# Kernel tuning notes

Measured on AMD Instinct MI355X. Metric: run time of the kernel, lower is better.

## Reference

```python
import jax, jax.numpy as jnp
import numpy as np

RATIO = 0.95
EPS = 1e-8
BIDIRECTIONAL = True


def _normalize_desc(fmap):
    # fmap: [1, ch, h, w] -> [h*w, ch], L2-normalized rows
    ch = fmap.shape[1]
    d = fmap.reshape(ch, -1).T
    return d / jnp.sqrt(jnp.sum(jnp.square(d), axis=1, keepdims=True))


def setup_inputs() -> dict:
    key = jax.random.key(0)
    k1, k2 = jax.random.split(key)
    map_A = jax.random.normal(k1, (1, 512, 96, 128), dtype=jnp.float32)
    map_B = jax.random.normal(k2, (1, 512, 96, 128), dtype=jnp.float32)
    return {"map_A": map_A, "map_B": map_B}


def reference(map_A, map_B):
    d1 = _normalize_desc(map_A)  # [N1, ch]
    d2 = _normalize_desc(map_B)  # [N2, ch]

    sim = d1 @ d2.T  # [N1, N2]

    # A -> B: top-2 over columns
    nns_sim12, nns12 = jax.lax.top_k(sim, 2)
    nns_dist12 = 2.0 - 2.0 * nns_sim12
    ratios12 = nns_dist12[:, 0] / (nns_dist12[:, 1] + EPS)
    nn12 = nns12[:, 0]
    match_sim = nns_sim12[:, 0]

    # B -> A: top-2 over rows of sim (columns of sim.T)
    nns_sim21, nns21 = jax.lax.top_k(sim.T, 2)
    nns_dist21 = 2.0 - 2.0 * nns_sim21
    ratios21 = nns_dist21[:, 0] / (nns_dist21[:, 1] + EPS)
    nn21 = nns21[:, 0]
    if not BIDIRECTIONAL:
        ratios21 = ratios21 * 0.0

    ids1 = jnp.arange(sim.shape[0])
    mask = (ids1 == nn21[nn12]) & (ratios12 <= RATIO) & (ratios21[nn12] <= RATIO)

    masked_sim = jnp.where(mask, match_sim, 0.0)
    return masked_sim, nn12, mask
```

## Files before the change

### kernel.cpp

```cpp
#include <hip/hip_runtime.h>
#include <stdint.h>

#define N      12288
#define CH     512
#define NTILE  96
#define NS     8
#define JT_PER_S 12
#define GPJ    16
#define NSTEP  (JT_PER_S * GPJ)

typedef _Float16 f16x8 __attribute__((ext_vector_type(8)));
typedef float    f32x4 __attribute__((ext_vector_type(4)));

struct Top2 { float v0, v1; int i0, i1; };

__device__ float g_invA[N];
__device__ float g_invB[N];
__device__ unsigned short g_AT[(size_t)N * 1024];
__device__ unsigned short g_BT[(size_t)N * 1024];
__device__ Top2  g_rpart[NS][N];
__device__ Top2  g_cpart[NTILE][N];
__device__ int   g_nn12[N];
__device__ float g_r12[N];
__device__ float g_sim0[N];
__device__ int   g_nn21[N];
__device__ float g_r21[N];

__device__ __forceinline__ void t2_ins(float v, int idx,
                                       float& v0, int& i0, float& v1, int& i1) {
  bool beats0 = (v > v0) || (v == v0 && idx < i0);
  bool beats1 = (v > v1) || (v == v1 && idx < i1);
  if (beats0) { v1 = v0; i1 = i0; v0 = v; i0 = idx; }
  else if (beats1) { v1 = v; i1 = idx; }
}

__device__ __forceinline__ float bf16_quant(float f) {
  unsigned int u = __float_as_uint(f);
  unsigned int r = 0x7fffu + ((u >> 16) & 1u);
  unsigned int q = ((u + r) >> 16) << 16;
  return __uint_as_float(q);
}

__global__ __launch_bounds__(256)
void prep_kernel(const float* __restrict__ A, const float* __restrict__ B) {
  const int d0 = blockIdx.x * 64;
  const float* src = blockIdx.y ? B : A;
  unsigned short* dst = blockIdx.y ? g_BT : g_AT;
  float* inv = blockIdx.y ? g_invB : g_invA;

  __shared__ float Ls[32][68];
  __shared__ unsigned short Os[64][64];
  __shared__ float Ps[4][64];

  const int t = threadIdx.x;
  const int a = t >> 6, dl = t & 63;
  float sum = 0.f;

  for (int g = 0; g < 16; ++g) {
    __syncthreads();
    {
      const int c = t >> 3, dc = (t & 7) * 8;
      const float* p = src + (size_t)(g * 32 + c) * N + d0 + dc;
      float4 v0 = *reinterpret_cast<const float4*>(p);
      float4 v1 = *reinterpret_cast<const float4*>(p + 4);
      *reinterpret_cast<float4*>(&Ls[c][dc])     = v0;
      *reinterpret_cast<float4*>(&Ls[c][dc + 4]) = v1;
    }
    __syncthreads();
    {
      _Float16 hv[8] __attribute__((aligned(16)));
      _Float16 lv[8] __attribute__((aligned(16)));
#pragma unroll
      for (int j = 0; j < 8; ++j) {
        float v = Ls[a * 8 + j][dl] * 1024.0f;
        sum += v * v;
        _Float16 h = (_Float16)v;
        float rr = v - (float)h;
        hv[j] = h;
        lv[j] = (_Float16)rr;
      }
      *reinterpret_cast<uint4*>(&Os[dl][a * 8])      = *reinterpret_cast<const uint4*>(hv);
      *reinterpret_cast<uint4*>(&Os[dl][32 + a * 8]) = *reinterpret_cast<const uint4*>(lv);
    }
    __syncthreads();
    {
#pragma unroll
      for (int p2 = 0; p2 < 2; ++p2) {
        const int d = p2 * 32 + (t >> 3), ch = t & 7;
        const int sc = ch ^ (d & 7);
        *reinterpret_cast<uint4*>((char*)dst
            + ((size_t)g * N + d0 + d) * 128 + sc * 16)
            = *reinterpret_cast<const uint4*>(&Os[d][ch * 8]);
      }
    }
  }
  Ps[a][dl] = sum;
  __syncthreads();
  if (t < 64) {
    float tot = Ps[0][t] + Ps[1][t] + Ps[2][t] + Ps[3][t];
    inv[d0 + t] = 1.0f / sqrtf(tot);
  }
}

__global__ __launch_bounds__(512, 4)
void sim_top2_mfma() {
  __shared__ unsigned short SM[2][2][128 * 64];
  __shared__ Top2 rowW[2][128];
  __shared__ Top2 colW[4][128];
  __shared__ float iaS[128];
  __shared__ float ibS[128];

  const int itile = blockIdx.x, slice = blockIdx.y;
  const int i0 = itile * 128;
  const int tid = threadIdx.x;
  const int wave = tid >> 6, lane = tid & 63;
  const int wr = wave & 3, wc = wave >> 2;
  const int fr = lane & 15, kq = lane >> 4;
  const int jtb = slice * JT_PER_S;

  const int tid2 = tid & 255;
  const char* opBase = (const char*)(wc ? g_BT : g_AT);

  uint4 s0, s1, s2, s3;
  auto issue = [&](int t) {
    const int gg = t & 15;
    const size_t rb = wc ? (size_t)(jtb + (t >> 4)) * 128 : (size_t)i0;
    const char* base = opBase + ((size_t)gg * N + rb) * 128 + tid2 * 16;
    s0 = *reinterpret_cast<const uint4*>(base);
    s1 = *reinterpret_cast<const uint4*>(base + 4096);
    s2 = *reinterpret_cast<const uint4*>(base + 8192);
    s3 = *reinterpret_cast<const uint4*>(base + 12288);
  };

  issue(0);

  if (tid < 128) {
    iaS[tid] = g_invA[i0 + tid];
    Top2 z; z.v0 = -1e30f; z.v1 = -1e30f; z.i0 = 0x7fffffff; z.i1 = 0x7fffffff;
    rowW[0][tid] = z; rowW[1][tid] = z;
  }

  const int f7 = fr & 7;
  const int cHi = (kq ^ f7) << 4;
  const int cLo = ((kq + 4) ^ f7) << 4;
  int aOff[2], bOff[4];
#pragma unroll
  for (int mi = 0; mi < 2; ++mi) aOff[mi] = (wr * 32 + mi * 16 + fr) * 128;
#pragma unroll
  for (int ni = 0; ni < 4; ++ni) bOff[ni] = (wc * 64 + ni * 16 + fr) * 128;

  char* const SMb = (char*)&SM[0][0][0];
  char* const wbase0 = SMb + wc * 16384 + tid2 * 16;

  int t = 0;
  for (int jt = jtb; jt < jtb + JT_PER_S; ++jt) {
    const int j0 = jt * 128;
    if (tid < 128) ibS[tid] = g_invB[j0 + tid];

    f32x4 acc[2][4];
#pragma unroll
    for (int mi = 0; mi < 2; ++mi)
#pragma unroll
      for (int ni = 0; ni < 4; ++ni)
#pragma unroll
        for (int q = 0; q < 4; ++q) acc[mi][ni][q] = 0.f;

    for (int g = 0; g < GPJ; ++g, ++t) {
      const int par = t & 1;
      __syncthreads();
      {
        char* wb = wbase0 + par * 32768;
        *reinterpret_cast<uint4*>(wb)          = s0;
        *reinterpret_cast<uint4*>(wb + 4096)   = s1;
        *reinterpret_cast<uint4*>(wb + 8192)   = s2;
        *reinterpret_cast<uint4*>(wb + 12288)  = s3;
      }
      if (t + 1 < NSTEP) issue(t + 1);
      __syncthreads();

      const char* bA = SMb + par * 32768;
      const char* bB = bA + 16384;
      f16x8 ah[2], al[2];
#pragma unroll
      for (int mi = 0; mi < 2; ++mi) {
        ah[mi] = *reinterpret_cast<const f16x8*>(bA + aOff[mi] + cHi);
        al[mi] = *reinterpret_cast<const f16x8*>(bA + aOff[mi] + cLo);
      }
#pragma unroll
      for (int ni = 0; ni < 4; ++ni) {
        f16x8 bh = *reinterpret_cast<const f16x8*>(bB + bOff[ni] + cHi);
        f16x8 bl = *reinterpret_cast<const f16x8*>(bB + bOff[ni] + cLo);
#pragma unroll
        for (int mi = 0; mi < 2; ++mi) {
          acc[mi][ni] = __builtin_amdgcn_mfma_f32_16x16x32_f16(ah[mi], bh, acc[mi][ni], 0, 0, 0);
          acc[mi][ni] = __builtin_amdgcn_mfma_f32_16x16x32_f16(ah[mi], bl, acc[mi][ni], 0, 0, 0);
          acc[mi][ni] = __builtin_amdgcn_mfma_f32_16x16x32_f16(al[mi], bh, acc[mi][ni], 0, 0, 0);
        }
      }
    }

    float ib[4];
#pragma unroll
    for (int ni = 0; ni < 4; ++ni) ib[ni] = ibS[wc * 64 + ni * 16 + fr];
#pragma unroll
    for (int mi = 0; mi < 2; ++mi)
#pragma unroll
      for (int r = 0; r < 4; ++r) {
        const float iar = iaS[wr * 32 + mi * 16 + kq * 4 + r];
#pragma unroll
        for (int ni = 0; ni < 4; ++ni)
          acc[mi][ni][r] *= iar * ib[ni];
      }

#pragma unroll
    for (int mi = 0; mi < 2; ++mi) {
#pragma unroll
      for (int r = 0; r < 4; ++r) {
        const int row = wr * 32 + mi * 16 + kq * 4 + r;
        float v0 = -1e30f, v1 = -1e30f; int id0 = 0x7fffffff, id1 = 0x7fffffff;
#pragma unroll
        for (int ni = 0; ni < 4; ++ni)
          t2_ins(acc[mi][ni][r], j0 + wc * 64 + ni * 16 + fr, v0, id0, v1, id1);
#pragma unroll
        for (int m = 1; m < 16; m <<= 1) {
          float ov0 = __shfl_xor(v0, m), ov1 = __shfl_xor(v1, m);
          int oi0 = __shfl_xor(id0, m), oi1 = __shfl_xor(id1, m);
          t2_ins(ov0, oi0, v0, id0, v1, id1);
          t2_ins(ov1, oi1, v0, id0, v1, id1);
        }
        if (fr == 0) {
          Top2 tT = rowW[wc][row];
          t2_ins(v0, id0, tT.v0, tT.i0, tT.v1, tT.i1);
          t2_ins(v1, id1, tT.v0, tT.i0, tT.v1, tT.i1);
          rowW[wc][row] = tT;
        }
      }
    }

#pragma unroll
    for (int ni = 0; ni < 4; ++ni) {
      float v0 = -1e30f, v1 = -1e30f; int id0 = 0x7fffffff, id1 = 0x7fffffff;
#pragma unroll
      for (int mi = 0; mi < 2; ++mi)
#pragma unroll
        for (int r = 0; r < 4; ++r)
          t2_ins(acc[mi][ni][r], i0 + wr * 32 + mi * 16 + kq * 4 + r, v0, id0, v1, id1);
#pragma unroll
      for (int m = 16; m < 64; m <<= 1) {
        float ov0 = __shfl_xor(v0, m), ov1 = __shfl_xor(v1, m);
        int oi0 = __shfl_xor(id0, m), oi1 = __shfl_xor(id1, m);
        t2_ins(ov0, oi0, v0, id0, v1, id1);
        t2_ins(ov1, oi1, v0, id0, v1, id1);
      }
      if (kq == 0) {
        Top2 tT; tT.v0 = v0; tT.v1 = v1; tT.i0 = id0; tT.i1 = id1;
        colW[wr][wc * 64 + ni * 16 + fr] = tT;
      }
    }
    __syncthreads();
    if (tid < 128) {
      Top2 tT = colW[0][tid];
#pragma unroll
      for (int w = 1; w < 4; ++w) {
        Top2 o = colW[w][tid];
        t2_ins(o.v0, o.i0, tT.v0, tT.i0, tT.v1, tT.i1);
        t2_ins(o.v1, o.i1, tT.v0, tT.i0, tT.v1, tT.i1);
      }
      g_cpart[itile][j0 + tid] = tT;
    }
  }

  __syncthreads();
  if (tid < 128) {
    Top2 tT = rowW[0][tid];
    Top2 o  = rowW[1][tid];
    t2_ins(o.v0, o.i0, tT.v0, tT.i0, tT.v1, tT.i1);
    t2_ins(o.v1, o.i1, tT.v0, tT.i0, tT.v1, tT.i1);
    g_rpart[slice][i0 + tid] = tT;
  }
}

__global__ void merge_kernel() {
  int i = blockIdx.x * 256 + threadIdx.x;
  if (i >= N) return;
  {
    float v0 = -1e30f, v1 = -1e30f; int id0 = 0x7fffffff, id1 = 0x7fffffff;
#pragma unroll
    for (int s = 0; s < NS; ++s) {
      Top2 p = g_rpart[s][i];
      t2_ins(p.v0, p.i0, v0, id0, v1, id1);
      t2_ins(p.v1, p.i1, v0, id0, v1, id1);
    }
    float d0 = 2.f - 2.f * v0, d1 = 2.f - 2.f * v1;
    g_nn12[i] = id0; g_r12[i] = d0 / (d1 + 1e-8f); g_sim0[i] = v0;
  }
  {
    float v0 = -1e30f, v1 = -1e30f; int id0 = 0x7fffffff, id1 = 0x7fffffff;
    for (int it = 0; it < NTILE; ++it) {
      Top2 p = g_cpart[it][i];
      t2_ins(p.v0, p.i0, v0, id0, v1, id1);
      t2_ins(p.v1, p.i1, v0, id0, v1, id1);
    }
    float d0 = 2.f - 2.f * v0, d1 = 2.f - 2.f * v1;
    g_nn21[i] = id0; g_r21[i] = d0 / (d1 + 1e-8f);
  }
}

__global__ void finalize_kernel(float* __restrict__ out) {
  int i = blockIdx.x * 256 + threadIdx.x;
  if (i >= N) return;
  int j = g_nn12[i];
  int jc = j < 0 ? 0 : (j >= N ? N - 1 : j);
  bool mask = (g_nn21[jc] == i) && (g_r12[i] <= 0.95f) && (g_r21[jc] <= 0.95f);
  out[i]         = bf16_quant(mask ? g_sim0[i] : 0.f);
  out[N + i]     = bf16_quant((float)j);
  out[2 * N + i] = mask ? 1.f : 0.f;
}

extern "C" void kernel_launch(void* const* d_in, const int* in_sizes, int n_in,
                              void* d_out, int out_size, void* d_ws, size_t ws_size,
                              hipStream_t stream) {
  const float* A = (const float*)d_in[0];
  const float* B = (const float*)d_in[1];
  (void)d_ws; (void)ws_size;

  prep_kernel<<<dim3(192, 2), 256, 0, stream>>>(A, B);
  sim_top2_mfma<<<dim3(NTILE, NS), 512, 0, stream>>>();
  merge_kernel<<<dim3((N + 255) / 256), 256, 0, stream>>>();
  finalize_kernel<<<dim3((N + 255) / 256), 256, 0, stream>>>((float*)d_out);
}
```

Baseline: 2.449 ms.

## Deepen global prefetch to two stages and remap blocks for L2 locality

Splits the register staging into two alternating sets so global loads for step t+2 are issued while step t is being consumed, which doubles the number of loads in flight. It replaces __syncthreads with raw s_barrier plus an explicit lgkmcnt wait so the barrier does not also wait on outstanding global loads. It also remaps block IDs so blocks that run together share A tiles and slices, to improve L2 reuse. In exchange the kernel holds extra VGPRs for the second staging set, which may reduce occupancy under the 512x4 launch bounds, and the hand-written barrier handling is easier to get wrong.

```diff
diff --git a/kernel.cpp b/kernel.cpp
--- a/kernel.cpp
+++ b/kernel.cpp
@@ -110,7 +110,9 @@
   __shared__ float iaS[128];
   __shared__ float ibS[128];
 
-  const int itile = blockIdx.x, slice = blockIdx.y;
+  const int bid = blockIdx.x + NTILE * blockIdx.y;
+  const int itile = (bid & 7) * 12 + ((bid >> 3) % 12);
+  const int slice = bid / NTILE;
   const int i0 = itile * 128;
   const int tid = threadIdx.x;
   const int wave = tid >> 6, lane = tid & 63;
@@ -121,24 +123,36 @@
   const int tid2 = tid & 255;
   const char* opBase = (const char*)(wc ? g_BT : g_AT);
 
-  uint4 s0, s1, s2, s3;
-  auto issue = [&](int t) {
+  uint4 sa0, sa1, sa2, sa3;
+  uint4 sb0, sb1, sb2, sb3;
+  auto issueA = [&](int t) {
     const int gg = t & 15;
     const size_t rb = wc ? (size_t)(jtb + (t >> 4)) * 128 : (size_t)i0;
     const char* base = opBase + ((size_t)gg * N + rb) * 128 + tid2 * 16;
-    s0 = *reinterpret_cast<const uint4*>(base);
-    s1 = *reinterpret_cast<const uint4*>(base + 4096);
-    s2 = *reinterpret_cast<const uint4*>(base + 8192);
-    s3 = *reinterpret_cast<const uint4*>(base + 12288);
+    sa0 = *reinterpret_cast<const uint4*>(base);
+    sa1 = *reinterpret_cast<const uint4*>(base + 4096);
+    sa2 = *reinterpret_cast<const uint4*>(base + 8192);
+    sa3 = *reinterpret_cast<const uint4*>(base + 12288);
   };
-
-  issue(0);
+  auto issueB = [&](int t) {
+    const int gg = t & 15;
+    const size_t rb = wc ? (size_t)(jtb + (t >> 4)) * 128 : (size_t)i0;
+    const char* base = opBase + ((size_t)gg * N + rb) * 128 + tid2 * 16;
+    sb0 = *reinterpret_cast<const uint4*>(base);
+    sb1 = *reinterpret_cast<const uint4*>(base + 4096);
+    sb2 = *reinterpret_cast<const uint4*>(base + 8192);
+    sb3 = *reinterpret_cast<const uint4*>(base + 12288);
+  };
 
   if (tid < 128) {
     iaS[tid] = g_invA[i0 + tid];
     Top2 z; z.v0 = -1e30f; z.v1 = -1e30f; z.i0 = 0x7fffffff; z.i1 = 0x7fffffff;
     rowW[0][tid] = z; rowW[1][tid] = z;
   }
+  __syncthreads();
+
+  issueA(0);
+  issueB(1);
 
   const int f7 = fr & 7;
   const int cHi = (kq ^ f7) << 4;
@@ -152,6 +166,44 @@
   char* const SMb = (char*)&SM[0][0][0];
   char* const wbase0 = SMb + wc * 16384 + tid2 * 16;
 
+#define KSTEP(PAR, S0, S1, S2, S3, ISSUE, TT)                                 \
+  {                                                                           \
+    __builtin_amdgcn_s_barrier();                                             \
+    asm volatile("" ::: "memory");                                            \
+    {                                                                         \
+      char* wb = wbase0 + (PAR) * 32768;                                      \
+      *reinterpret_cast<uint4*>(wb)         = S0;                             \
+      *reinterpret_cast<uint4*>(wb + 4096)  = S1;                             \
+      *reinterpret_cast<uint4*>(wb + 8192)  = S2;                             \
+      *reinterpret_cast<uint4*>(wb + 12288) = S3;                             \
+    }                                                                         \
+    if ((TT) + 2 < NSTEP) ISSUE((TT) + 2);                                    \
+    asm volatile("s_waitcnt lgkmcnt(0)" ::: "memory");                        \
+    __builtin_amdgcn_s_barrier();                                             \
+    asm volatile("" ::: "memory");                                            \
+    {                                                                         \
+      const char* bA = SMb + (PAR) * 32768;                                   \
+      const char* bB = bA + 16384;                                            \
+      f16x8 ah[2], al[2];                                                     \
+      _Pragma("unroll")                                                       \
+      for (int mi = 0; mi < 2; ++mi) {                                        \
+        ah[mi] = *reinterpret_cast<const f16x8*>(bA + aOff[mi] + cHi);        \
+        al[mi] = *reinterpret_cast<const f16x8*>(bA + aOff[mi] + cLo);        \
+      }                                                                       \
+      _Pragma("unroll")                                                       \
+      for (int ni = 0; ni < 4; ++ni) {                                        \
+        f16x8 bh = *reinterpret_cast<const f16x8*>(bB + bOff[ni] + cHi);      \
+        f16x8 bl = *reinterpret_cast<const f16x8*>(bB + bOff[ni] + cLo);      \
+        _Pragma("unroll")                                                     \
+        for (int mi = 0; mi < 2; ++mi) {                                      \
+          acc[mi][ni] = __builtin_amdgcn_mfma_f32_16x16x32_f16(ah[mi], bh, acc[mi][ni], 0, 0, 0); \
+          acc[mi][ni] = __builtin_amdgcn_mfma_f32_16x16x32_f16(ah[mi], bl, acc[mi][ni], 0, 0, 0); \
+          acc[mi][ni] = __builtin_amdgcn_mfma_f32_16x16x32_f16(al[mi], bh, acc[mi][ni], 0, 0, 0); \
+        }                                                                     \
+      }                                                                       \
+    }                                                                         \
+  }
+
   int t = 0;
   for (int jt = jtb; jt < jtb + JT_PER_S; ++jt) {
     const int j0 = jt * 128;
@@ -165,38 +217,11 @@
 #pragma unroll
         for (int q = 0; q < 4; ++q) acc[mi][ni][q] = 0.f;
 
-    for (int g = 0; g < GPJ; ++g, ++t) {
-      const int par = t & 1;
-      __syncthreads();
-      {
-        char* wb = wbase0 + par * 32768;
-        *reinterpret_cast<uint4*>(wb)          = s0;
-        *reinterpret_cast<uint4*>(wb + 4096)   = s1;
-        *reinterpret_cast<uint4*>(wb + 8192)   = s2;
-        *reinterpret_cast<uint4*>(wb + 12288)  = s3;
-      }
-      if (t + 1 < NSTEP) issue(t + 1);
-      __syncthreads();
-
-      const char* bA = SMb + par * 32768;
-      const char* bB = bA + 16384;
-      f16x8 ah[2], al[2];
-#pragma unroll
-      for (int mi = 0; mi < 2; ++mi) {
-        ah[mi] = *reinterpret_cast<const f16x8*>(bA + aOff[mi] + cHi);
-        al[mi] = *reinterpret_cast<const f16x8*>(bA + aOff[mi] + cLo);
-      }
-#pragma unroll
-      for (int ni = 0; ni < 4; ++ni) {
-        f16x8 bh = *reinterpret_cast<const f16x8*>(bB + bOff[ni] + cHi);
-        f16x8 bl = *reinterpret_cast<const f16x8*>(bB + bOff[ni] + cLo);
-#pragma unroll
-        for (int mi = 0; mi < 2; ++mi) {
-          acc[mi][ni] = __builtin_amdgcn_mfma_f32_16x16x32_f16(ah[mi], bh, acc[mi][ni], 0, 0, 0);
-          acc[mi][ni] = __builtin_amdgcn_mfma_f32_16x16x32_f16(ah[mi], bl, acc[mi][ni], 0, 0, 0);
-          acc[mi][ni] = __builtin_amdgcn_mfma_f32_16x16x32_f16(al[mi], bh, acc[mi][ni], 0, 0, 0);
-        }
-      }
+    for (int g2 = 0; g2 < GPJ / 2; ++g2) {
+      KSTEP(0, sa0, sa1, sa2, sa3, issueA, t);
+      ++t;
+      KSTEP(1, sb0, sb1, sb2, sb3, issueB, t);
+      ++t;
     }
 
     float ib[4];
@@ -269,6 +294,7 @@
       g_cpart[itile][j0 + tid] = tT;
     }
   }
+#undef KSTEP
 
   __syncthreads();
   if (tid < 128) {
```

Result: no change. 2.434 ms (-0.6%).

## Enlarge similarity GEMM tiles to 256x256 with dynamic shared memory

Applied to the files above, without the earlier changes.

Grows the per-block output tile from 128x128 to 256x256. Each wave now owns a 128x64 sub-tile with 32 accumulators, so every LDS fragment feeds more MFMAs and operand traffic per flop drops. The grid is rearranged to 48x16 with a swizzled itile order, shared memory moves to a 154 KB dynamic allocation, and the syncs become raw s_barrier calls with explicit lgkmcnt waits. In exchange, register pressure rises to 128 fp32 accumulators per lane, occupancy falls to launch_bounds 2, and there are fewer blocks to cover the CUs.

```diff
diff --git a/kernel.cpp b/kernel.cpp
--- a/kernel.cpp
+++ b/kernel.cpp
@@ -3,11 +3,13 @@
 
 #define N      12288
 #define CH     512
-#define NTILE  96
-#define NS     8
-#define JT_PER_S 12
+#define TI2    256
+#define NT2    48
+#define NS2    16
+#define JT2    3
 #define GPJ    16
-#define NSTEP  (JT_PER_S * GPJ)
+#define NSTEP2 (JT2 * GPJ)
+#define DSMEM_BYTES (131072 + 16384 + 8192 + 2048)
 
 typedef _Float16 f16x8 __attribute__((ext_vector_type(8)));
 typedef float    f32x4 __attribute__((ext_vector_type(4)));
@@ -18,8 +20,8 @@
 __device__ float g_invB[N];
 __device__ unsigned short g_AT[(size_t)N * 1024];
 __device__ unsigned short g_BT[(size_t)N * 1024];
-__device__ Top2  g_rpart[NS][N];
-__device__ Top2  g_cpart[NTILE][N];
+__device__ Top2  g_rpart[NS2][N];
+__device__ Top2  g_cpart[NT2][N];
 __device__ int   g_nn12[N];
 __device__ float g_r12[N];
 __device__ float g_sim0[N];
@@ -102,125 +104,143 @@
   }
 }
 
-__global__ __launch_bounds__(512, 4)
+__global__ __launch_bounds__(512, 2)
 void sim_top2_mfma() {
-  __shared__ unsigned short SM[2][2][128 * 64];
-  __shared__ Top2 rowW[2][128];
-  __shared__ Top2 colW[4][128];
-  __shared__ float iaS[128];
-  __shared__ float ibS[128];
-
-  const int itile = blockIdx.x, slice = blockIdx.y;
-  const int i0 = itile * 128;
+  extern __shared__ char smem[];
+  char* const SMb = smem;
+  Top2* const rowW = (Top2*)(smem + 131072);
+  Top2* const colW = (Top2*)(smem + 131072 + 16384);
+  float* const iaS = (float*)(smem + 131072 + 16384 + 8192);
+  float* const ibS = iaS + 256;
+
+  const int q = blockIdx.x;
+  const int itile = (q & 7) * 6 + (q >> 3);
+  const int slice = blockIdx.y;
+  const int i0 = itile * TI2;
   const int tid = threadIdx.x;
   const int wave = tid >> 6, lane = tid & 63;
-  const int wr = wave & 3, wc = wave >> 2;
+  const int wr = wave & 1, wc = wave >> 1;
   const int fr = lane & 15, kq = lane >> 4;
-  const int jtb = slice * JT_PER_S;
-
+  const int jtb = slice * JT2;
+
+  const int side = wave >> 2;
   const int tid2 = tid & 255;
-  const char* opBase = (const char*)(wc ? g_BT : g_AT);
-
-  uint4 s0, s1, s2, s3;
+  const char* opBase = (const char*)(side ? g_BT : g_AT);
+
+  uint4 s0, s1, s2, s3, s4, s5, s6, s7;
   auto issue = [&](int t) {
     const int gg = t & 15;
-    const size_t rb = wc ? (size_t)(jtb + (t >> 4)) * 128 : (size_t)i0;
+    const size_t rb = side ? (size_t)(jtb + (t >> 4)) * TI2 : (size_t)i0;
     const char* base = opBase + ((size_t)gg * N + rb) * 128 + tid2 * 16;
     s0 = *reinterpret_cast<const uint4*>(base);
     s1 = *reinterpret_cast<const uint4*>(base + 4096);
     s2 = *reinterpret_cast<const uint4*>(base + 8192);
     s3 = *reinterpret_cast<const uint4*>(base + 12288);
+    s4 = *reinterpret_cast<const uint4*>(base + 16384);
+    s5 = *reinterpret_cast<const uint4*>(base + 20480);
+    s6 = *reinterpret_cast<const uint4*>(base + 24576);
+    s7 = *reinterpret_cast<const uint4*>(base + 28672);
   };
 
   issue(0);
 
-  if (tid < 128) {
+  if (tid < 256) {
     iaS[tid] = g_invA[i0 + tid];
     Top2 z; z.v0 = -1e30f; z.v1 = -1e30f; z.i0 = 0x7fffffff; z.i1 = 0x7fffffff;
-    rowW[0][tid] = z; rowW[1][tid] = z;
-  }
+#pragma unroll
+    for (int w = 0; w < 4; ++w) rowW[w * 256 + tid] = z;
+  }
+  __syncthreads();
 
   const int f7 = fr & 7;
   const int cHi = (kq ^ f7) << 4;
   const int cLo = ((kq + 4) ^ f7) << 4;
-  int aOff[2], bOff[4];
-#pragma unroll
-  for (int mi = 0; mi < 2; ++mi) aOff[mi] = (wr * 32 + mi * 16 + fr) * 128;
-#pragma unroll
-  for (int ni = 0; ni < 4; ++ni) bOff[ni] = (wc * 64 + ni * 16 + fr) * 128;
-
-  char* const SMb = (char*)&SM[0][0][0];
-  char* const wbase0 = SMb + wc * 16384 + tid2 * 16;
+  const int aOff0 = (wr * 128 + fr) * 128;
+  const int bOff0 = (wc * 64 + fr) * 128;
+  char* const wbase0 = SMb + side * 32768 + tid2 * 16;
 
   int t = 0;
-  for (int jt = jtb; jt < jtb + JT_PER_S; ++jt) {
-    const int j0 = jt * 128;
-    if (tid < 128) ibS[tid] = g_invB[j0 + tid];
-
-    f32x4 acc[2][4];
-#pragma unroll
-    for (int mi = 0; mi < 2; ++mi)
+  for (int jt = jtb; jt < jtb + JT2; ++jt) {
+    const int j0 = jt * TI2;
+    if (tid < 256) ibS[tid] = g_invB[j0 + tid];
+
+    f32x4 acc[8][4];
+#pragma unroll
+    for (int mi = 0; mi < 8; ++mi)
 #pragma unroll
       for (int ni = 0; ni < 4; ++ni)
 #pragma unroll
-        for (int q = 0; q < 4; ++q) acc[mi][ni][q] = 0.f;
+        for (int e = 0; e < 4; ++e) acc[mi][ni][e] = 0.f;
 
     for (int g = 0; g < GPJ; ++g, ++t) {
       const int par = t & 1;
-      __syncthreads();
+      __builtin_amdgcn_s_barrier();
+      asm volatile("" ::: "memory");
       {
-        char* wb = wbase0 + par * 32768;
+        char* wb = wbase0 + par * 65536;
         *reinterpret_cast<uint4*>(wb)          = s0;
         *reinterpret_cast<uint4*>(wb + 4096)   = s1;
         *reinterpret_cast<uint4*>(wb + 8192)   = s2;
         *reinterpret_cast<uint4*>(wb + 12288)  = s3;
-      }
-      if (t + 1 < NSTEP) issue(t + 1);
-      __syncthreads();
-
-      const char* bA = SMb + par * 32768;
-      const char* bB = bA + 16384;
-      f16x8 ah[2], al[2];
-#pragma unroll
-      for (int mi = 0; mi < 2; ++mi) {
-        ah[mi] = *reinterpret_cast<const f16x8*>(bA + aOff[mi] + cHi);
-        al[mi] = *reinterpret_cast<const f16x8*>(bA + aOff[mi] + cLo);
-      }
-#pragma unroll
-      for (int ni = 0; ni < 4; ++ni) {
-        f16x8 bh = *reinterpret_cast<const f16x8*>(bB + bOff[ni] + cHi);
-        f16x8 bl = *reinterpret_cast<const f16x8*>(bB + bOff[ni] + cLo);
-#pragma unroll
-        for (int mi = 0; mi < 2; ++mi) {
-          acc[mi][ni] = __builtin_amdgcn_mfma_f32_16x16x32_f16(ah[mi], bh, acc[mi][ni], 0, 0, 0);
-          acc[mi][ni] = __builtin_amdgcn_mfma_f32_16x16x32_f16(ah[mi], bl, acc[mi][ni], 0, 0, 0);
-          acc[mi][ni] = __builtin_amdgcn_mfma_f32_16x16x32_f16(al[mi], bh, acc[mi][ni], 0, 0, 0);
+        *reinterpret_cast<uint4*>(wb + 16384)  = s4;
+        *reinterpret_cast<uint4*>(wb + 20480)  = s5;
+        *reinterpret_cast<uint4*>(wb + 24576)  = s6;
+        *reinterpret_cast<uint4*>(wb + 28672)  = s7;
+      }
+      if (t + 1 < NSTEP2) issue(t + 1);
+      asm volatile("s_waitcnt lgkmcnt(0)" ::: "memory");
+      __builtin_amdgcn_s_barrier();
+      __builtin_amdgcn_sched_barrier(0);
+
+      const char* bA = SMb + par * 65536;
+      const char* bB = bA + 32768;
+#pragma unroll
+      for (int h = 0; h < 2; ++h) {
+        f16x8 ah[4], al[4];
+#pragma unroll
+        for (int m = 0; m < 4; ++m) {
+          const char* pa = bA + aOff0 + (h * 4 + m) * 2048;
+          ah[m] = *reinterpret_cast<const f16x8*>(pa + cHi);
+          al[m] = *reinterpret_cast<const f16x8*>(pa + cLo);
         }
-      }
+#pragma unroll
+        for (int ni = 0; ni < 4; ++ni) {
+          const char* pb = bB + bOff0 + ni * 2048;
+          f16x8 bh = *reinterpret_cast<const f16x8*>(pb + cHi);
+          f16x8 bl = *reinterpret_cast<const f16x8*>(pb + cLo);
+#pragma unroll
+          for (int m = 0; m < 4; ++m) {
+            acc[h*4+m][ni] = __builtin_amdgcn_mfma_f32_16x16x32_f16(ah[m], bh, acc[h*4+m][ni], 0, 0, 0);
+            acc[h*4+m][ni] = __builtin_amdgcn_mfma_f32_16x16x32_f16(ah[m], bl, acc[h*4+m][ni], 0, 0, 0);
+            acc[h*4+m][ni] = __builtin_amdgcn_mfma_f32_16x16x32_f16(al[m], bh, acc[h*4+m][ni], 0, 0, 0);
+          }
+        }
+      }
+      asm volatile("" ::: "memory");
     }
 
     float ib[4];
 #pragma unroll
     for (int ni = 0; ni < 4; ++ni) ib[ni] = ibS[wc * 64 + ni * 16 + fr];
 #pragma unroll
-    for (int mi = 0; mi < 2; ++mi)
-#pragma unroll
-      for (int r = 0; r < 4; ++r) {
-        const float iar = iaS[wr * 32 + mi * 16 + kq * 4 + r];
+    for (int mi = 0; mi < 8; ++mi)
+#pragma unroll
+      for (int e = 0; e < 4; ++e) {
+        const float iar = iaS[wr * 128 + mi * 16 + kq * 4 + e];
 #pragma unroll
         for (int ni = 0; ni < 4; ++ni)
-          acc[mi][ni][r] *= iar * ib[ni];
-      }
-
-#pragma unroll
-    for (int mi = 0; mi < 2; ++mi) {
-#pragma unroll
-      for (int r = 0; r < 4; ++r) {
-        const int row = wr * 32 + mi * 16 + kq * 4 + r;
+          acc[mi][ni][e] *= iar * ib[ni];
+      }
+
+#pragma unroll
+    for (int mi = 0; mi < 8; ++mi) {
+#pragma unroll
+      for (int e = 0; e < 4; ++e) {
+        const int row = wr * 128 + mi * 16 + kq * 4 + e;
         float v0 = -1e30f, v1 = -1e30f; int id0 = 0x7fffffff, id1 = 0x7fffffff;
 #pragma unroll
         for (int ni = 0; ni < 4; ++ni)
-          t2_ins(acc[mi][ni][r], j0 + wc * 64 + ni * 16 + fr, v0, id0, v1, id1);
+          t2_ins(acc[mi][ni][e], j0 + wc * 64 + ni * 16 + fr, v0, id0, v1, id1);
 #pragma unroll
         for (int m = 1; m < 16; m <<= 1) {
           float ov0 = __shfl_xor(v0, m), ov1 = __shfl_xor(v1, m);
@@ -229,10 +249,10 @@
           t2_ins(ov1, oi1, v0, id0, v1, id1);
         }
         if (fr == 0) {
-          Top2 tT = rowW[wc][row];
+          Top2 tT = rowW[wc * 256 + row];
           t2_ins(v0, id0, tT.v0, tT.i0, tT.v1, tT.i1);
           t2_ins(v1, id1, tT.v0, tT.i0, tT.v1, tT.i1);
-          rowW[wc][row] = tT;
+          rowW[wc * 256 + row] = tT;
         }
       }
     }
@@ -241,10 +261,10 @@
     for (int ni = 0; ni < 4; ++ni) {
       float v0 = -1e30f, v1 = -1e30f; int id0 = 0x7fffffff, id1 = 0x7fffffff;
 #pragma unroll
-      for (int mi = 0; mi < 2; ++mi)
-#pragma unroll
-        for (int r = 0; r < 4; ++r)
-          t2_ins(acc[mi][ni][r], i0 + wr * 32 + mi * 16 + kq * 4 + r, v0, id0, v1, id1);
+      for (int mi = 0; mi < 8; ++mi)
+#pragma unroll
+        for (int e = 0; e < 4; ++e)
+          t2_ins(acc[mi][ni][e], i0 + wr * 128 + mi * 16 + kq * 4 + e, v0, id0, v1, id1);
 #pragma unroll
       for (int m = 16; m < 64; m <<= 1) {
         float ov0 = __shfl_xor(v0, m), ov1 = __shfl_xor(v1, m);
@@ -254,28 +274,28 @@
       }
       if (kq == 0) {
         Top2 tT; tT.v0 = v0; tT.v1 = v1; tT.i0 = id0; tT.i1 = id1;
-        colW[wr][wc * 64 + ni * 16 + fr] = tT;
+        colW[wr * 256 + wc * 64 + ni * 16 + fr] = tT;
       }
     }
     __syncthreads();
-    if (tid < 128) {
-      Top2 tT = colW[0][tid];
-#pragma unroll
-      for (int w = 1; w < 4; ++w) {
-        Top2 o = colW[w][tid];
-        t2_ins(o.v0, o.i0, tT.v0, tT.i0, tT.v1, tT.i1);
-        t2_ins(o.v1, o.i1, tT.v0, tT.i0, tT.v1, tT.i1);
-      }
+    if (tid < 256) {
+      Top2 tT = colW[tid];
+      Top2 o  = colW[256 + tid];
+      t2_ins(o.v0, o.i0, tT.v0, tT.i0, tT.v1, tT.i1);
+      t2_ins(o.v1, o.i1, tT.v0, tT.i0, tT.v1, tT.i1);
       g_cpart[itile][j0 + tid] = tT;
     }
   }
 
   __syncthreads();
-  if (tid < 128) {
-    Top2 tT = rowW[0][tid];
-    Top2 o  = rowW[1][tid];
-    t2_ins(o.v0, o.i0, tT.v0, tT.i0, tT.v1, tT.i1);
-    t2_ins(o.v1, o.i1, tT.v0, tT.i0, tT.v1, tT.i1);
+  if (tid < 256) {
+    Top2 tT = rowW[tid];
+#pragma unroll
+    for (int w = 1; w < 4; ++w) {
+      Top2 o = rowW[w * 256 + tid];
+      t2_ins(o.v0, o.i0, tT.v0, tT.i0, tT.v1, tT.i1);
+      t2_ins(o.v1, o.i1, tT.v0, tT.i0, tT.v1, tT.i1);
+    }
     g_rpart[slice][i0 + tid] = tT;
   }
 }
@@ -286,7 +306,7 @@
   {
     float v0 = -1e30f, v1 = -1e30f; int id0 = 0x7fffffff, id1 = 0x7fffffff;
 #pragma unroll
-    for (int s = 0; s < NS; ++s) {
+    for (int s = 0; s < NS2; ++s) {
       Top2 p = g_rpart[s][i];
       t2_ins(p.v0, p.i0, v0, id0, v1, id1);
       t2_ins(p.v1, p.i1, v0, id0, v1, id1);
@@ -296,7 +316,7 @@
   }
   {
     float v0 = -1e30f, v1 = -1e30f; int id0 = 0x7fffffff, id1 = 0x7fffffff;
-    for (int it = 0; it < NTILE; ++it) {
+    for (int it = 0; it < NT2; ++it) {
       Top2 p = g_cpart[it][i];
       t2_ins(p.v0, p.i0, v0, id0, v1, id1);
       t2_ins(p.v1, p.i1, v0, id0, v1, id1);
@@ -324,8 +344,15 @@
   const float* B = (const float*)d_in[1];
   (void)d_ws; (void)ws_size;
 
+  static bool attr_done = false;
+  if (!attr_done) {
+    hipFuncSetAttribute(reinterpret_cast<const void*>(sim_top2_mfma),
+                        hipFuncAttributeMaxDynamicSharedMemorySize, DSMEM_BYTES);
+    attr_done = true;
+  }
+
   prep_kernel<<<dim3(192, 2), 256, 0, stream>>>(A, B);
-  sim_top2_mfma<<<dim3(NTILE, NS), 512, 0, stream>>>();
+  sim_top2_mfma<<<dim3(NT2, NS2), 512, DSMEM_BYTES, stream>>>();
   merge_kernel<<<dim3((N + 255) / 256), 256, 0, stream>>>();
   finalize_kernel<<<dim3((N + 255) / 256), 256, 0, stream>>>((float*)d_out);
 }
```

New measurement: 3.029 ms. 1.24x slower.
